# Kernel tuning notes

Hardware: AMD Instinct MI355X
Metric: run time of the kernel (lower is better)

Reference implementation:

```python
import jax, jax.numpy as jnp
import numpy as np
import math

N = 100000
E = 1600000
D = 256          # input_size
H = 64           # head_size = input_size // n_heads = 256 // 4


def setup_inputs() -> dict:
    key = jax.random.key(0)
    k1, k2, k3, k4, k5 = jax.random.split(key, 5)
    X = jax.random.normal(k1, (N, D), dtype=jnp.float32)
    edge_index = jax.random.randint(k2, (2, E), 0, N, dtype=jnp.int64)
    # Linear(input_size, head_size, bias=False) weights, stored as [D, H] so Q = X @ Wq
    s = 1.0 / math.sqrt(D)
    Wq = jax.random.uniform(k3, (D, H), dtype=jnp.float32, minval=-s, maxval=s)
    Wk = jax.random.uniform(k4, (D, H), dtype=jnp.float32, minval=-s, maxval=s)
    Wv = jax.random.uniform(k5, (D, H), dtype=jnp.float32, minval=-s, maxval=s)
    return {"X": X, "Wq": Wq, "Wk": Wk, "Wv": Wv, "edge_index": edge_index}


def reference(X, Wq, Wk, Wv, edge_index):
    dk = math.sqrt(H)
    Q = X @ Wq  # [N, H]
    K = X @ Wk
    V = X @ Wv
    src = edge_index[0]  # row of sparse matrix -> softmax segment (dim=1 softmax)
    dst = edge_index[1]  # column -> neighbor supplying K/V
    scores = jnp.sum(Q[src] * K[dst], axis=-1) / dk  # [E]
    # per-row (per src node) stable softmax over edges
    m = jax.ops.segment_max(scores, src, num_segments=N)          # [N], -inf for empty rows
    m = jnp.where(jnp.isfinite(m), m, 0.0)
    e = jnp.exp(scores - m[src])                                   # [E]
    denom = jax.ops.segment_sum(e, src, num_segments=N)            # [N]
    alpha = e / jnp.maximum(denom[src], 1e-38)                     # [E]
    # scatter-weighted V aggregation: out[i] = sum_{(i,j) in edges} alpha_ij * V[j]
    out = jax.ops.segment_sum(alpha[:, None] * V[dst], src, num_segments=N)  # [N, H]
    return out
```

## Files before the change

### kernel.cpp

```cpp
#include <hip/hip_runtime.h>

typedef unsigned short u16;
typedef unsigned int u32;
typedef short short8 __attribute__((ext_vector_type(8)));
typedef float f32x4 __attribute__((ext_vector_type(4)));
typedef u32 u32x4 __attribute__((ext_vector_type(4)));

__device__ __forceinline__ u16 f2bf(float f) {
    union { float f; u32 i; } c; c.f = f;
    u32 i = c.i;
    return (u16)((i + 0x7FFFu + ((i >> 16) & 1u)) >> 16);
}
__device__ __forceinline__ float bf2f(u16 u) {
    union { u32 i; float f; } c; c.i = ((u32)u) << 16; return c.f;
}
__device__ __forceinline__ void bf2x(u32 p, float& lo, float& hi) {
    union { u32 i; float f; } a, b;
    a.i = p << 16; b.i = p & 0xFFFF0000u;
    lo = a.f; hi = b.f;
}
__device__ __forceinline__ u32 cvtpk_bf16(float lo, float hi) {
    u32 r;
    asm("v_cvt_pk_bf16_f32 %0, %1, %2" : "=v"(r) : "v"(lo), "v"(hi));
    return r;
}

__global__ void wfrag_kernel(const float* __restrict__ Wq,
                             const float* __restrict__ Wk,
                             const float* __restrict__ Wv,
                             u16* __restrict__ wf)
{
    int idx = blockIdx.x * 256 + threadIdx.x;
    if (idx >= 12 * 8 * 64) return;
    int lane = idx & 63;
    int s = (idx >> 6) & 7;
    int t = idx >> 9;
    int n = t * 16 + (lane & 15);
    const float* Wsrc = (n < 64) ? Wq : ((n < 128) ? Wk : Wv);
    int col = n & 63;
    int kbase = s * 32 + (lane >> 4) * 8;
    u16 o[8];
#pragma unroll
    for (int j = 0; j < 8; ++j) o[j] = f2bf(Wsrc[(size_t)(kbase + j) * 64 + col]);
    *(short8*)(wf + (size_t)idx * 8) = *(const short8*)o;
}

#define TM 32
__global__ __launch_bounds__(256, 2) void qkv_mfma(
    const float* __restrict__ X, const u16* __restrict__ wf,
    float* __restrict__ Qs, u16* __restrict__ KVsb,
    int N, int NT)
{
    __shared__ float xs[TM * 256];

    const int tid  = threadIdx.x;
    const int lane = tid & 63;
    const int wave = tid >> 6;
    const int m    = lane & 15;
    const int quad = lane >> 4;
    const int t0   = wave * 3;

    const short8* wfp = (const short8*)wf;
    short8 bfr0[8], bfr1[8], bfr2[8];
#pragma unroll
    for (int s = 0; s < 8; ++s) {
        bfr0[s] = wfp[(size_t)((t0 + 0) * 8 + s) * 64 + lane];
        bfr1[s] = wfp[(size_t)((t0 + 1) * 8 + s) * 64 + lane];
        bfr2[s] = wfp[(size_t)((t0 + 2) * 8 + s) * 64 + lane];
    }

    for (int tile = blockIdx.x; tile < NT; tile += gridDim.x) {
#pragma unroll
        for (int it = 0; it < 8; ++it) {
            int c0  = (it * 4 + wave) * 64;
            int c   = c0 + lane;
            int row = c >> 6;
            int sblk = (c & 63) ^ (row & 7);
            int arow = tile * TM + row;
            if (arow >= N) arow = N - 1;
            const float* g = X + (size_t)arow * 256 + sblk * 4;
            float* l = xs + c0 * 4;
            __builtin_amdgcn_global_load_lds(
                (const __attribute__((address_space(1))) void*)g,
                (__attribute__((address_space(3))) void*)l, 16, 0, 0);
        }
        __syncthreads();

        f32x4 acc[2][3];
#pragma unroll
        for (int rb = 0; rb < 2; ++rb)
#pragma unroll
            for (int tt = 0; tt < 3; ++tt) acc[rb][tt] = (f32x4)0.f;

#pragma unroll
        for (int rb = 0; rb < 2; ++rb) {
            const int row = rb * 16 + m;
            const float* xrow = xs + row * 256;
            const int sw = m & 7;
#pragma unroll
            for (int s = 0; s < 8; ++s) {
                int B0 = quad * 2 + s * 8;
                float4 a0 = *(const float4*)(xrow + ((B0)     ^ sw) * 4);
                float4 a1 = *(const float4*)(xrow + ((B0 + 1) ^ sw) * 4);
                union { u32x4 u; short8 s8; } af;
                af.u.x = cvtpk_bf16(a0.x, a0.y);
                af.u.y = cvtpk_bf16(a0.z, a0.w);
                af.u.z = cvtpk_bf16(a1.x, a1.y);
                af.u.w = cvtpk_bf16(a1.z, a1.w);
                acc[rb][0] = __builtin_amdgcn_mfma_f32_16x16x32_bf16(af.s8, bfr0[s], acc[rb][0], 0, 0, 0);
                acc[rb][1] = __builtin_amdgcn_mfma_f32_16x16x32_bf16(af.s8, bfr1[s], acc[rb][1], 0, 0, 0);
                acc[rb][2] = __builtin_amdgcn_mfma_f32_16x16x32_bf16(af.s8, bfr2[s], acc[rb][2], 0, 0, 0);
            }
        }

#pragma unroll
        for (int rb = 0; rb < 2; ++rb) {
            int rbase = tile * TM + rb * 16 + quad * 4;
#pragma unroll
            for (int tt = 0; tt < 3; ++tt) {
                int t = t0 + tt;
                int col = (t & 3) * 16 + m;
#pragma unroll
                for (int r = 0; r < 4; ++r) {
                    int rr = rbase + r;
                    if (rr >= N) continue;
                    float v = acc[rb][tt][r];
                    if (t < 4)      Qs  [(size_t)rr * 64  + col]      = v;
                    else if (t < 8) KVsb[(size_t)rr * 128 + col]      = f2bf(v);
                    else            KVsb[(size_t)rr * 128 + 64 + col] = f2bf(v);
                }
            }
        }
        __syncthreads();
    }
}


__global__ __launch_bounds__(256) void count_kernel(
    const int* __restrict__ src, int* __restrict__ bsize,
    int E, int N, int NB, int chunk)
{
    __shared__ int cnt[512];
    for (int i = threadIdx.x; i < 512; i += 256) cnt[i] = 0;
    __syncthreads();
    int lo = blockIdx.x * chunk;
    int hi = min(E, lo + chunk);
    for (int e = lo + (int)threadIdx.x; e < hi; e += 256) {
        int s = src[e];
        if ((unsigned)s < (unsigned)N) atomicAdd(&cnt[s >> 8], 1);
    }
    __syncthreads();
    for (int b = threadIdx.x; b < NB; b += 256)
        if (cnt[b]) atomicAdd(&bsize[b], cnt[b]);
}

__global__ __launch_bounds__(512) void scan391_kernel(
    const int* __restrict__ bsize, int* __restrict__ bbase,
    int* __restrict__ cursor, int* __restrict__ row_ptr_N, int NB)
{
    __shared__ int sd[512];
    int t = threadIdx.x;
    int v = (t < NB) ? bsize[t] : 0;
    sd[t] = v;
    __syncthreads();
    for (int off = 1; off < 512; off <<= 1) {
        int x = (t >= off) ? sd[t - off] : 0;
        __syncthreads();
        sd[t] += x;
        __syncthreads();
    }
    if (t < NB) {
        int excl = sd[t] - v;
        bbase[t] = excl;
        cursor[t] = excl;
        if (t == NB - 1) {
            bbase[NB] = sd[t];
            *row_ptr_N = sd[t];
        }
    }
}

__global__ __launch_bounds__(256) void scatter_pairs_kernel(
    const int* __restrict__ src, const int* __restrict__ dst,
    int* __restrict__ cursor, int2* __restrict__ pairs,
    int E, int N, int NB, int chunk)
{
    __shared__ int cnt[512];
    __shared__ int basei[512];
    for (int i = threadIdx.x; i < 512; i += 256) cnt[i] = 0;
    __syncthreads();
    int lo = blockIdx.x * chunk;
    int hi = min(E, lo + chunk);
    for (int e = lo + (int)threadIdx.x; e < hi; e += 256) {
        int s = src[e];
        if ((unsigned)s < (unsigned)N) atomicAdd(&cnt[s >> 8], 1);
    }
    __syncthreads();
    for (int b = threadIdx.x; b < NB; b += 256)
        basei[b] = cnt[b] ? atomicAdd(&cursor[b], cnt[b]) : 0;
    __syncthreads();
    for (int i = threadIdx.x; i < 512; i += 256) cnt[i] = 0;
    __syncthreads();
    for (int e = lo + (int)threadIdx.x; e < hi; e += 256) {
        int s = src[e];
        if ((unsigned)s >= (unsigned)N) continue;
        int d = dst[e];
        if ((unsigned)d >= (unsigned)N) d = 0;
        int bk = s >> 8;
        int p = basei[bk] + atomicAdd(&cnt[bk], 1);
        pairs[p] = make_int2(s, d);
    }
}

#define MAXB 6144
__global__ __launch_bounds__(256) void sort_bucket_kernel(
    const int2* __restrict__ pairs, const int* __restrict__ bbase,
    int* __restrict__ row_ptr, int* __restrict__ sorted_dst, int N)
{
    __shared__ int deg[256];
    __shared__ int off[256];
    __shared__ int cur[256];
    __shared__ int ldst[MAXB];

    int bk = blockIdx.x;
    int n0 = bk * 256;
    int nn = min(256, N - n0);
    int base = bbase[bk];
    int size = bbase[bk + 1] - base;
    int t = threadIdx.x;

    deg[t] = 0;
    __syncthreads();
    for (int i = t; i < size; i += 256)
        atomicAdd(&deg[pairs[base + i].x & 255], 1);
    __syncthreads();
    off[t] = deg[t];
    __syncthreads();
    for (int s = 1; s < 256; s <<= 1) {
        int x = (t >= s) ? off[t - s] : 0;
        __syncthreads();
        off[t] += x;
        __syncthreads();
    }
    int excl = off[t] - deg[t];
    cur[t] = excl;
    if (t < nn) row_ptr[n0 + t] = base + excl;
    __syncthreads();
    int cap = min(size, MAXB);
    for (int i = t; i < size; i += 256) {
        int2 pr = pairs[base + i];
        int p = atomicAdd(&cur[pr.x & 255], 1);
        if (p < MAXB) ldst[p] = pr.y;
    }
    __syncthreads();
    for (int i = t; i < cap; i += 256)
        sorted_dst[base + i] = ldst[i];
    for (int i = cap + t; i < size; i += 256)
        sorted_dst[base + i] = 0;
}

__global__ __launch_bounds__(256) void attn_csr(
    const float* __restrict__ Qs, const u16* __restrict__ KVsb,
    const int* __restrict__ row_ptr, const int* __restrict__ sdst,
    float* __restrict__ out, int N)
{
    int sg = (int)((blockIdx.x * 256 + threadIdx.x) >> 3);
    if (sg >= N) return;
    int sl = threadIdx.x & 7;

    const float* qp = Qs + (size_t)sg * 64 + sl * 8;
    float4 q0 = *(const float4*)(qp);
    float4 q1 = *(const float4*)(qp + 4);

    int beg = row_ptr[sg];
    int end = row_ptr[sg + 1];

    float l = 0.f;
    float a0 = 0.f, a1 = 0.f, a2 = 0.f, a3 = 0.f;
    float a4 = 0.f, a5 = 0.f, a6 = 0.f, a7 = 0.f;

    if (beg < end) {
        const int last = end - 1;
        uint4 kr[4], vr[4];
        int pd[4];

#pragma unroll
        for (int i = 0; i < 4; ++i) {
            int e = beg + i;
            int d = sdst[e <= last ? e : last];
            const u16* kv = KVsb + (size_t)d * 128 + sl * 8;
            kr[i] = *(const uint4*)(kv);
            vr[i] = *(const uint4*)(kv + 64);
            int ep = beg + 4 + i;
            pd[i] = sdst[ep <= last ? ep : last];
        }

        for (int base = beg; base < end; base += 4) {
#pragma unroll
            for (int i = 0; i < 4; ++i) {
                int e = base + i;
                uint4 k = kr[i], v = vr[i];

                {
                    const u16* kv = KVsb + (size_t)pd[i] * 128 + sl * 8;
                    kr[i] = *(const uint4*)(kv);
                    vr[i] = *(const uint4*)(kv + 64);
                    int ep = e + 8;
                    pd[i] = sdst[ep <= last ? ep : last];
                }

                float k0, k1, k2, k3, k4, k5, k6, k7;
                bf2x(k.x, k0, k1); bf2x(k.y, k2, k3);
                bf2x(k.z, k4, k5); bf2x(k.w, k6, k7);

                float p = q0.x * k0 + q0.y * k1 + q0.z * k2 + q0.w * k3
                        + q1.x * k4 + q1.y * k5 + q1.z * k6 + q1.w * k7;
                p += __shfl_xor(p, 1);
                p += __shfl_xor(p, 2);
                p += __shfl_xor(p, 4);

                float pe = __expf(p * 0.125f);

                float v0, v1, v2, v3, v4, v5, v6, v7;
                bf2x(v.x, v0, v1); bf2x(v.y, v2, v3);
                bf2x(v.z, v4, v5); bf2x(v.w, v6, v7);

                if (e < end) {
                    l += pe;
                    a0 += pe * v0; a1 += pe * v1; a2 += pe * v2; a3 += pe * v3;
                    a4 += pe * v4; a5 += pe * v5; a6 += pe * v6; a7 += pe * v7;
                }
            }
        }
    }

    float inv = (l > 0.f) ? (1.f / l) : 0.f;
    float* op = out + (size_t)sg * 64 + sl * 8;
    *(float4*)(op)     = make_float4(a0 * inv, a1 * inv, a2 * inv, a3 * inv);
    *(float4*)(op + 4) = make_float4(a4 * inv, a5 * inv, a6 * inv, a7 * inv);
}

extern "C" void kernel_launch(void* const* d_in, const int* in_sizes, int n_in,
                              void* d_out, int out_size, void* d_ws, size_t ws_size,
                              hipStream_t stream)
{
    const float* X  = (const float*)d_in[0];
    const float* Wq = (const float*)d_in[1];
    const float* Wk = (const float*)d_in[2];
    const float* Wv = (const float*)d_in[3];
    const int*   ei = (const int*)d_in[4];

    const int N = in_sizes[0] / 256;
    const int E = in_sizes[4] / 2;
    const int* src = ei;
    const int* dst = ei + E;
    const int NB = (N + 255) >> 8;

    char* w = (char*)d_ws;
    float* Qs = (float*)w;      w += (size_t)N * 64 * sizeof(float);
    u16* KVsb = (u16*)w;        w += (size_t)N * 128 * sizeof(u16);
    int2* pairs = (int2*)w;     w += (size_t)E * sizeof(int2);
    int* sorted_dst = (int*)w;  w += (size_t)E * sizeof(int);
    int* row_ptr = (int*)w;     w += (size_t)(N + 1) * sizeof(int);
    int* bsize = (int*)w;       w += (size_t)(NB + 1) * sizeof(int);
    int* bbase = (int*)w;       w += (size_t)(NB + 1) * sizeof(int);
    int* cursor = (int*)w;      w += (size_t)(NB + 1) * sizeof(int);
    u16* wf = (u16*)w;          w += (size_t)12 * 8 * 64 * 8 * sizeof(u16);

    hipMemsetAsync(bsize, 0, (size_t)(NB + 1) * sizeof(int), stream);

    const int B1 = 160;
    const int chunk = (E + B1 - 1) / B1;
    const int NT = (N + TM - 1) / TM;

    wfrag_kernel<<<24, 256, 0, stream>>>(Wq, Wk, Wv, wf);
    qkv_mfma<<<768, 256, 0, stream>>>(X, wf, Qs, KVsb, N, NT);

    count_kernel<<<B1, 256, 0, stream>>>(src, bsize, E, N, NB, chunk);
    scan391_kernel<<<1, 512, 0, stream>>>(bsize, bbase, cursor, row_ptr + N, NB);
    scatter_pairs_kernel<<<B1, 256, 0, stream>>>(src, dst, cursor, pairs, E, N, NB, chunk);
    sort_bucket_kernel<<<NB, 256, 0, stream>>>(pairs, bbase, row_ptr, sorted_dst, N);

    attn_csr<<<(N * 8 + 255) / 256, 256, 0, stream>>>(
        Qs, KVsb, row_ptr, sorted_dst, (float*)d_out, N);
}
```

Before: 330.4 us.

## Build CSR with per-node global atomics instead of two-level bucket sort

Replaces the bucketed counting sort (per-256-node buckets with shared-memory histograms, a pair scatter, then a per-bucket local sort) with a direct CSR build. A per-node degree count using global atomics is followed by a three-kernel multi-block scan and a scatter that places each edge through a global atomic cursor per source node. This drops the intermediate pairs buffer and the bucket sort pass. In exchange it issues 1.6M contended global atomics twice, launches more kernels, and edge order within a row is no longer deterministic.

```diff
diff --git a/kernel.cpp b/kernel.cpp
--- a/kernel.cpp
+++ b/kernel.cpp
@@ -136,31 +136,25 @@
 }
 
 
-__global__ __launch_bounds__(256) void count_kernel(
-    const int* __restrict__ src, int* __restrict__ bsize,
-    int E, int N, int NB, int chunk)
-{
-    __shared__ int cnt[512];
-    for (int i = threadIdx.x; i < 512; i += 256) cnt[i] = 0;
-    __syncthreads();
-    int lo = blockIdx.x * chunk;
-    int hi = min(E, lo + chunk);
-    for (int e = lo + (int)threadIdx.x; e < hi; e += 256) {
+__global__ __launch_bounds__(256) void deg_kernel(
+    const int* __restrict__ src, int* __restrict__ deg, int E, int N)
+{
+    int i = blockIdx.x * 256 + threadIdx.x;
+    int stride = gridDim.x * 256;
+    for (int e = i; e < E; e += stride) {
         int s = src[e];
-        if ((unsigned)s < (unsigned)N) atomicAdd(&cnt[s >> 8], 1);
-    }
-    __syncthreads();
-    for (int b = threadIdx.x; b < NB; b += 256)
-        if (cnt[b]) atomicAdd(&bsize[b], cnt[b]);
-}
-
-__global__ __launch_bounds__(512) void scan391_kernel(
-    const int* __restrict__ bsize, int* __restrict__ bbase,
-    int* __restrict__ cursor, int* __restrict__ row_ptr_N, int NB)
+        if ((unsigned)s < (unsigned)N) atomicAdd(&deg[s], 1);
+    }
+}
+
+__global__ __launch_bounds__(512) void scanA_kernel(
+    const int* __restrict__ deg, int* __restrict__ pref,
+    int* __restrict__ bsum, int N)
 {
     __shared__ int sd[512];
     int t = threadIdx.x;
-    int v = (t < NB) ? bsize[t] : 0;
+    int i = blockIdx.x * 512 + t;
+    int v = (i < N) ? deg[i] : 0;
     sd[t] = v;
     __syncthreads();
     for (int off = 1; off < 512; off <<= 1) {
@@ -169,94 +163,55 @@
         sd[t] += x;
         __syncthreads();
     }
-    if (t < NB) {
-        int excl = sd[t] - v;
-        bbase[t] = excl;
-        cursor[t] = excl;
-        if (t == NB - 1) {
-            bbase[NB] = sd[t];
-            *row_ptr_N = sd[t];
-        }
-    }
-}
-
-__global__ __launch_bounds__(256) void scatter_pairs_kernel(
+    if (i < N) pref[i] = sd[t] - v;
+    if (t == 511) bsum[blockIdx.x] = sd[511];
+}
+
+__global__ __launch_bounds__(256) void scanB_kernel(
+    const int* __restrict__ bsum, int* __restrict__ boff,
+    int* __restrict__ row_ptr_N, int NBlk)
+{
+    __shared__ int sd[256];
+    int t = threadIdx.x;
+    int v = (t < NBlk) ? bsum[t] : 0;
+    sd[t] = v;
+    __syncthreads();
+    for (int off = 1; off < 256; off <<= 1) {
+        int x = (t >= off) ? sd[t - off] : 0;
+        __syncthreads();
+        sd[t] += x;
+        __syncthreads();
+    }
+    if (t < NBlk) boff[t] = sd[t] - v;
+    if (t == NBlk - 1) *row_ptr_N = sd[t];
+}
+
+__global__ __launch_bounds__(512) void scanC_kernel(
+    const int* __restrict__ pref, const int* __restrict__ boff,
+    int* __restrict__ row_ptr, int* __restrict__ cursor, int N)
+{
+    int i = blockIdx.x * 512 + threadIdx.x;
+    if (i < N) {
+        int v = pref[i] + boff[blockIdx.x];
+        row_ptr[i] = v;
+        cursor[i] = v;
+    }
+}
+
+__global__ __launch_bounds__(256) void scatter_kernel(
     const int* __restrict__ src, const int* __restrict__ dst,
-    int* __restrict__ cursor, int2* __restrict__ pairs,
-    int E, int N, int NB, int chunk)
-{
-    __shared__ int cnt[512];
-    __shared__ int basei[512];
-    for (int i = threadIdx.x; i < 512; i += 256) cnt[i] = 0;
-    __syncthreads();
-    int lo = blockIdx.x * chunk;
-    int hi = min(E, lo + chunk);
-    for (int e = lo + (int)threadIdx.x; e < hi; e += 256) {
-        int s = src[e];
-        if ((unsigned)s < (unsigned)N) atomicAdd(&cnt[s >> 8], 1);
-    }
-    __syncthreads();
-    for (int b = threadIdx.x; b < NB; b += 256)
-        basei[b] = cnt[b] ? atomicAdd(&cursor[b], cnt[b]) : 0;
-    __syncthreads();
-    for (int i = threadIdx.x; i < 512; i += 256) cnt[i] = 0;
-    __syncthreads();
-    for (int e = lo + (int)threadIdx.x; e < hi; e += 256) {
+    int* __restrict__ cursor, int* __restrict__ sorted_dst, int E, int N)
+{
+    int i = blockIdx.x * 256 + threadIdx.x;
+    int stride = gridDim.x * 256;
+    for (int e = i; e < E; e += stride) {
         int s = src[e];
         if ((unsigned)s >= (unsigned)N) continue;
         int d = dst[e];
         if ((unsigned)d >= (unsigned)N) d = 0;
-        int bk = s >> 8;
-        int p = basei[bk] + atomicAdd(&cnt[bk], 1);
-        pairs[p] = make_int2(s, d);
-    }
-}
-
-#define MAXB 6144
-__global__ __launch_bounds__(256) void sort_bucket_kernel(
-    const int2* __restrict__ pairs, const int* __restrict__ bbase,
-    int* __restrict__ row_ptr, int* __restrict__ sorted_dst, int N)
-{
-    __shared__ int deg[256];
-    __shared__ int off[256];
-    __shared__ int cur[256];
-    __shared__ int ldst[MAXB];
-
-    int bk = blockIdx.x;
-    int n0 = bk * 256;
-    int nn = min(256, N - n0);
-    int base = bbase[bk];
-    int size = bbase[bk + 1] - base;
-    int t = threadIdx.x;
-
-    deg[t] = 0;
-    __syncthreads();
-    for (int i = t; i < size; i += 256)
-        atomicAdd(&deg[pairs[base + i].x & 255], 1);
-    __syncthreads();
-    off[t] = deg[t];
-    __syncthreads();
-    for (int s = 1; s < 256; s <<= 1) {
-        int x = (t >= s) ? off[t - s] : 0;
-        __syncthreads();
-        off[t] += x;
-        __syncthreads();
-    }
-    int excl = off[t] - deg[t];
-    cur[t] = excl;
-    if (t < nn) row_ptr[n0 + t] = base + excl;
-    __syncthreads();
-    int cap = min(size, MAXB);
-    for (int i = t; i < size; i += 256) {
-        int2 pr = pairs[base + i];
-        int p = atomicAdd(&cur[pr.x & 255], 1);
-        if (p < MAXB) ldst[p] = pr.y;
-    }
-    __syncthreads();
-    for (int i = t; i < cap; i += 256)
-        sorted_dst[base + i] = ldst[i];
-    for (int i = cap + t; i < size; i += 256)
-        sorted_dst[base + i] = 0;
+        int pos = atomicAdd(&cursor[s], 1);
+        sorted_dst[pos] = d;
+    }
 }
 
 __global__ __launch_bounds__(256) void attn_csr(
@@ -354,32 +309,33 @@
     const int E = in_sizes[4] / 2;
     const int* src = ei;
     const int* dst = ei + E;
-    const int NB = (N + 255) >> 8;
+
+    const int NBlk = (N + 511) / 512;
 
     char* w = (char*)d_ws;
     float* Qs = (float*)w;      w += (size_t)N * 64 * sizeof(float);
     u16* KVsb = (u16*)w;        w += (size_t)N * 128 * sizeof(u16);
-    int2* pairs = (int2*)w;     w += (size_t)E * sizeof(int2);
     int* sorted_dst = (int*)w;  w += (size_t)E * sizeof(int);
     int* row_ptr = (int*)w;     w += (size_t)(N + 1) * sizeof(int);
-    int* bsize = (int*)w;       w += (size_t)(NB + 1) * sizeof(int);
-    int* bbase = (int*)w;       w += (size_t)(NB + 1) * sizeof(int);
-    int* cursor = (int*)w;      w += (size_t)(NB + 1) * sizeof(int);
+    int* deg = (int*)w;         w += (size_t)N * sizeof(int);
+    int* cursor = (int*)w;      w += (size_t)N * sizeof(int);
+    int* pref = (int*)w;        w += (size_t)N * sizeof(int);
+    int* bsum = (int*)w;        w += (size_t)(NBlk + 1) * sizeof(int);
+    int* boff = (int*)w;        w += (size_t)(NBlk + 1) * sizeof(int);
     u16* wf = (u16*)w;          w += (size_t)12 * 8 * 64 * 8 * sizeof(u16);
 
-    hipMemsetAsync(bsize, 0, (size_t)(NB + 1) * sizeof(int), stream);
-
-    const int B1 = 160;
-    const int chunk = (E + B1 - 1) / B1;
+    hipMemsetAsync(deg, 0, (size_t)N * sizeof(int), stream);
+
     const int NT = (N + TM - 1) / TM;
 
     wfrag_kernel<<<24, 256, 0, stream>>>(Wq, Wk, Wv, wf);
     qkv_mfma<<<768, 256, 0, stream>>>(X, wf, Qs, KVsb, N, NT);
 
-    count_kernel<<<B1, 256, 0, stream>>>(src, bsize, E, N, NB, chunk);
-    scan391_kernel<<<1, 512, 0, stream>>>(bsize, bbase, cursor, row_ptr + N, NB);
-    scatter_pairs_kernel<<<B1, 256, 0, stream>>>(src, dst, cursor, pairs, E, N, NB, chunk);
-    sort_bucket_kernel<<<NB, 256, 0, stream>>>(pairs, bbase, row_ptr, sorted_dst, N);
+    deg_kernel<<<2048, 256, 0, stream>>>(src, deg, E, N);
+    scanA_kernel<<<NBlk, 512, 0, stream>>>(deg, pref, bsum, N);
+    scanB_kernel<<<1, 256, 0, stream>>>(bsum, boff, row_ptr + N, NBlk);
+    scanC_kernel<<<NBlk, 512, 0, stream>>>(pref, boff, row_ptr, cursor, N);
+    scatter_kernel<<<2048, 256, 0, stream>>>(src, dst, cursor, sorted_dst, E, N);
 
     attn_csr<<<(N * 8 + 255) / 256, 256, 0, stream>>>(
         Qs, KVsb, row_ptr, sorted_dst, (float*)d_out, N);
```

Result: slower. 428.8 us (+29.8%).
